# Optimization experiments

Hardware: AMD Instinct MI355X
Metric: run time of the kernel (lower is better)

Reference implementation:

```python
import jax, jax.numpy as jnp
import numpy as np

K = 16  # knn


def conv1x1(x, w, b):
    # x: (B,Cin,k,N), w: (Cout,Cin), b: (Cout,)
    return jnp.einsum('oc,bckn->bokn', w, x) + b[None, :, None, None]


def leaky(x):
    return jnp.where(x >= 0, x, 0.2 * x)


def conv_res(x, sc_w, sc_b, a_w, a_b, b_w, b_b, c_w, c_b):
    sc = conv1x1(x, sc_w, sc_b)
    h = leaky(conv1x1(x, a_w, a_b))
    h = leaky(conv1x1(h, b_w, b_b))
    h = conv1x1(h, c_w, c_b)
    return h + sc


def get_knn_feature(xyz, k):
    # xyz: (B,3,N) -> feature (B,10,k,N)
    x_t = jnp.transpose(xyz, (0, 2, 1))  # (B,N,3)
    xx = jnp.sum(x_t * x_t, axis=-1)  # (B,N)
    inner = jnp.einsum('bnc,bmc->bnm', x_t, x_t)  # (B,N,N)
    d2 = xx[:, :, None] + xx[:, None, :] - 2.0 * inner  # squared dists
    _, idx = jax.lax.top_k(-d2, k)  # (B,N,k) nearest (includes self)
    neighbors = jax.vmap(lambda pts, i: pts[i])(x_t, idx)  # (B,N,k,3)
    center = x_t[:, :, None, :]  # (B,N,1,3)
    rel = neighbors - center
    dist = jnp.sqrt(jnp.sum(rel * rel, axis=-1, keepdims=True) + 1e-12)  # (B,N,k,1)
    feat = jnp.concatenate([jnp.broadcast_to(center, neighbors.shape), neighbors, rel, dist], axis=-1)  # (B,N,k,10)
    return jnp.transpose(feat, (0, 3, 2, 1))  # (B,10,k,N)


def _mk_w(key, o, i):
    s = 1.0 / np.sqrt(i)
    return jax.random.uniform(key, (o, i), jnp.float32, -s, s)


def setup_inputs():
    key = jax.random.key(0)
    ks = jax.random.split(key, 20)
    B, N = 4, 8192
    hide, out = 64, 128
    inp = {'xyz': jax.random.normal(ks[0], (B, 3, N), jnp.float32)}
    # CONV_Res(10, 64, 64)
    inp['p1_sc_w'] = _mk_w(ks[1], hide, 10); inp['p1_sc_b'] = jnp.zeros((hide,), jnp.float32)
    inp['p1_a_w'] = _mk_w(ks[2], hide, 10); inp['p1_a_b'] = jnp.zeros((hide,), jnp.float32)
    inp['p1_b_w'] = _mk_w(ks[3], hide, hide); inp['p1_b_b'] = jnp.zeros((hide,), jnp.float32)
    inp['p1_c_w'] = _mk_w(ks[4], hide, hide); inp['p1_c_b'] = jnp.zeros((hide,), jnp.float32)
    # CONV_Res(128, 64, 128)
    inp['p2_sc_w'] = _mk_w(ks[5], out, 2 * hide); inp['p2_sc_b'] = jnp.zeros((out,), jnp.float32)
    inp['p2_a_w'] = _mk_w(ks[6], hide, 2 * hide); inp['p2_a_b'] = jnp.zeros((hide,), jnp.float32)
    inp['p2_b_w'] = _mk_w(ks[7], out, hide); inp['p2_b_b'] = jnp.zeros((out,), jnp.float32)
    inp['p2_c_w'] = _mk_w(ks[8], out, out); inp['p2_c_b'] = jnp.zeros((out,), jnp.float32)
    return inp


def reference(xyz, p1_sc_w, p1_sc_b, p1_a_w, p1_a_b, p1_b_w, p1_b_b, p1_c_w, p1_c_b,
              p2_sc_w, p2_sc_b, p2_a_w, p2_a_b, p2_b_w, p2_b_b, p2_c_w, p2_c_b):
    x = get_knn_feature(xyz, K)  # (B,10,k,N)
    x = conv_res(x, p1_sc_w, p1_sc_b, p1_a_w, p1_a_b, p1_b_w, p1_b_b, p1_c_w, p1_c_b)  # (B,64,k,N)
    x1 = jnp.max(x, axis=2, keepdims=True)  # (B,64,1,N)
    x1 = jnp.broadcast_to(x1, x.shape)  # repeat over k
    x = jnp.concatenate([x, x1], axis=1)  # (B,128,k,N)
    x = conv_res(x, p2_sc_w, p2_sc_b, p2_a_w, p2_a_b, p2_b_w, p2_b_b, p2_c_w, p2_c_b)  # (B,128,k,N)
    return jnp.max(x, axis=2)  # (B,128,N)
```

## Files before the change

### kernel.cpp

```cpp
#include <hip/hip_runtime.h>
#include <hip/hip_bf16.h>

#define B_ 4
#define N_ 8192
#define KNN 16
#define BN_ (B_*N_)
#define NPOS (BN_*KNN)

typedef __attribute__((ext_vector_type(8))) short bf16x8;
typedef __attribute__((ext_vector_type(4))) float f32x4;

static __device__ __forceinline__ unsigned short f2bf(float f) {
  union { float f; unsigned u; } v; v.f = f;
  unsigned r = v.u + 0x7fff + ((v.u >> 16) & 1);
  return (unsigned short)(r >> 16);
}
static __device__ __forceinline__ float lk(float x) { return x >= 0.f ? x : 0.2f*x; }
static __device__ __forceinline__ unsigned pk2(float a, float b) {
  return (unsigned)f2bf(a) | ((unsigned)f2bf(b) << 16);
}

__global__ void k_prep(const float* __restrict__ xyz, float4* __restrict__ pts4) {
  int i = blockIdx.x * 256 + threadIdx.x;
  if (i >= BN_) return;
  int b = i >> 13, n = i & (N_-1);
  const float* p = xyz + b*3*N_;
  float x = p[n], y = p[N_+n], z = p[2*N_+n];
  float xx = fmaf(z, z, fmaf(y, y, x*x));
  pts4[i] = make_float4(x, y, z, xx);
}

__global__ void k_wcvt(const float* __restrict__ w_sc, const float* __restrict__ w_a,
                       const float* __restrict__ w_b, const float* __restrict__ w_c,
                       const float* __restrict__ p1a, const float* __restrict__ p1sc,
                       const float* __restrict__ p1b, const float* __restrict__ p1c,
                       unsigned short* __restrict__ out) {
  int i = blockIdx.x*256 + threadIdx.x;
  if (i >= 61440) return;
  if (i < 49152) {
    int x = i*2;
    const float* w; int base, K2;
    if (x < 32768)      { w = w_sc; base = 0;     K2 = 256; }
    else if (x < 49152) { w = w_a;  base = 32768; K2 = 256; }
    else if (x < 65536) { w = w_b;  base = 49152; K2 = 128; }
    else                { w = w_c;  base = 65536; K2 = 256; }
    int off = x - base;
    int row = off / K2;
    int colb = (off & (K2-1)) ^ ((row & 7) << 4);
    int k = colb >> 1;
    out[i] = f2bf(w[row*(K2 >> 1) + k]);
  } else {
    int e = i - 49152;
    float val; int byteoff;
    if (e < 2048) {
      int row = e >> 5, k = e & 31;
      val = (k < 10) ? p1a[row*10 + k] : 0.f;
      byteoff = row*64 + ((2*k) ^ ((row & 3) << 4));
    } else if (e < 4096) {
      int le = e - 2048, row = le >> 5, k = le & 31;
      val = (k < 10) ? p1sc[row*10 + k] : 0.f;
      byteoff = 4096 + row*64 + ((2*k) ^ ((row & 3) << 4));
    } else if (e < 8192) {
      int le = e - 4096, row = le >> 6, k = le & 63;
      val = p1b[row*64 + k];
      byteoff = 8192 + row*128 + ((2*k) ^ ((row & 7) << 4));
    } else {
      int le = e - 8192, row = le >> 6, k = le & 63;
      val = p1c[row*64 + k];
      byteoff = 16384 + row*128 + ((2*k) ^ ((row & 7) << 4));
    }
    out[49152 + (byteoff >> 1)] = f2bf(val);
  }
}

static __device__ __forceinline__ unsigned long long bitonic64(
    unsigned long long key, int lane) {
  #pragma unroll
  for (int size = 2; size <= 64; size <<= 1) {
    #pragma unroll
    for (int stride = size >> 1; stride >= 1; stride >>= 1) {
      unsigned long long ok = __shfl_xor((long long)key, stride);
      bool up = ((lane & size) == 0);
      bool keepmin = (((lane & stride) == 0) == up);
      bool oless = ok < key;
      if (oless == keepmin) key = ok;
    }
  }
  return key;
}

template<int U>
static __device__ __forceinline__ void scan_groups(
    const float4* __restrict__ cand, int itbase, int ch,
    float4 me, int lane,
    unsigned long long* __restrict__ bw,
    unsigned long long& topk, float& rhs, int& cnt) {
  float s[U]; int cid[U];
  #pragma unroll
  for (int u = 0; u < U; ++u) {
    int ci = (itbase + u)*64 + lane;
    float4 c = cand[ci];
    float dot = fmaf(me.z, c.z, fmaf(me.y, c.y, me.x*c.x));
    s[u] = fmaf(-2.0f, dot, c.w);
    cid[u] = ch*2048 + ci;
  }
  #pragma unroll
  for (int u = 0; u < U; ++u) {
    unsigned long long m = __ballot(s[u] < rhs);
    if (m) {
      int prefix = __builtin_amdgcn_mbcnt_hi((unsigned)(m >> 32),
                    __builtin_amdgcn_mbcnt_lo((unsigned)m, 0));
      if (s[u] < rhs) {
        float d2 = me.w + s[u];
        bw[cnt + prefix] =
          ((unsigned long long)__float_as_uint(d2) << 32) | (unsigned)cid[u];
      }
      cnt += __popcll(m);
      if (cnt >= 48) {
        int base = 0;
        while (cnt > 0) {
          int c2 = cnt > 48 ? 48 : cnt;
          unsigned long long e = (lane < 16) ? topk
            : ((lane - 16) < c2 ? bw[base + lane - 16] : ~0ull);
          topk = bitonic64(e, lane);
          base += c2; cnt -= c2;
        }
        unsigned long long k15 = __shfl((long long)topk, 15);
        rhs = __uint_as_float((unsigned)(k15 >> 32)) - me.w;
      }
    }
  }
}

__global__ __launch_bounds__(512) void k_knn(const float4* __restrict__ pts4,
                                             int* __restrict__ knn) {
  __shared__ float4 cand[2048];
  __shared__ unsigned long long buf[8][112];
  const int lane = threadIdx.x & 63;
  const int wv   = threadIdx.x >> 6;
  const int q = blockIdx.x * 8 + wv;
  const int b = q >> 13;
  const int n = q & (N_-1);
  const float4* __restrict__ P = pts4 + (b << 13);
  float4 me = P[n];

  unsigned long long topk = ~0ull;
  float rhs = __builtin_inff();
  int cnt = 0;
  unsigned long long* __restrict__ bw = buf[wv];

  for (int ch = 0; ch < 4; ++ch) {
    __syncthreads();
    #pragma unroll
    for (int t = 0; t < 4; ++t)
      cand[t*512 + threadIdx.x] = P[ch*2048 + t*512 + threadIdx.x];
    __syncthreads();

    if (ch == 0) {
      float4 c = cand[lane];
      float dot = fmaf(me.z, c.z, fmaf(me.y, c.y, me.x*c.x));
      float d2 = (me.w + c.w) - 2.0f*dot;
      unsigned long long key =
        ((unsigned long long)__float_as_uint(d2) << 32) | (unsigned)lane;
      topk = bitonic64(key, lane);
      unsigned long long k15 = __shfl((long long)topk, 15);
      rhs = __uint_as_float((unsigned)(k15 >> 32)) - me.w;
      scan_groups<3>(cand, 1, 0, me, lane, bw, topk, rhs, cnt);
      #pragma unroll 1
      for (int it = 4; it < 32; it += 4)
        scan_groups<4>(cand, it, 0, me, lane, bw, topk, rhs, cnt);
    } else {
      #pragma unroll 1
      for (int it = 0; it < 32; it += 4)
        scan_groups<4>(cand, it, ch, me, lane, bw, topk, rhs, cnt);
    }
  }
  {
    int base = 0;
    while (cnt > 0) {
      int c2 = cnt > 48 ? 48 : cnt;
      unsigned long long e = (lane < 16) ? topk
        : ((lane - 16) < c2 ? bw[base + lane - 16] : ~0ull);
      topk = bitonic64(e, lane);
      base += c2; cnt -= c2;
    }
  }
  if (lane < 16) knn[(q << 4) + lane] = (int)(unsigned)(topk & 0xffffffffu);
}

__global__ __launch_bounds__(512, 2) void k_p12(
    const float4* __restrict__ pts4, const int* __restrict__ knn,
    const unsigned short* __restrict__ wbf,
    const float* __restrict__ a_b1, const float* __restrict__ b_b1,
    const float* __restrict__ c_b1, const float* __restrict__ sc_b1,
    const float* __restrict__ sc_b2, const float* __restrict__ a_b2,
    const float* __restrict__ b_b2, const float* __restrict__ c_b2,
    float* __restrict__ out) {
  __shared__ __align__(16) unsigned short Ws1[12288];
  __shared__ __align__(16) unsigned short Ws2[49152];
  __shared__ __align__(16) unsigned short Hr[8][2304];
  const int tid = threadIdx.x;
  const int lane = tid & 63, wv = tid >> 6;
  const int colr = lane & 15, kq = lane >> 4;

  #pragma unroll
  for (int j = 0; j < 3; ++j)
    ((uint4*)Ws1)[j*512 + tid] = ((const uint4*)(wbf + 49152))[j*512 + tid];
  #pragma unroll
  for (int it = 0; it < 12; ++it)
    ((uint4*)Ws2)[it*512 + tid] = ((const uint4*)wbf)[it*512 + tid];

  const char* WS = (const char*)Ws1;
  const char* WSC = (const char*)Ws2;
  const char* WA  = (const char*)(Ws2 + 16384);
  const char* WB  = (const char*)(Ws2 + 24576);
  const char* WC  = (const char*)(Ws2 + 32768);
  char* H = (char*)Hr[wv];
  float (*outT)[16] = (float(*)[16])(&Hr[0][0]);

#define WF(base, row, K2, ksbyte) \
  (*(const bf16x8*)((base) + (row)*(K2) + ((((ksbyte) + kq*16)) ^ (((row)&7)<<4))))

  __syncthreads();

  for (int t = 0; t < 8; ++t) {
    const int bn0 = blockIdx.x*128 + t*16;

    unsigned short fb0[10], fb1[10];
    #pragma unroll
    for (int ct = 0; ct < 2; ++ct) {
      int bn = bn0 + wv*2 + ct;
      int b = bn >> 13;
      float4 cp = pts4[bn];
      int nid = knn[bn*16 + colr];
      float4 np = pts4[(b << 13) + nid];
      float rx = np.x - cp.x, ry = np.y - cp.y, rz = np.z - cp.z;
      float dist = sqrtf(fmaf(rz, rz, fmaf(ry, ry, rx*rx)) + 1e-12f);
      unsigned short* fb = ct ? fb1 : fb0;
      fb[0]=f2bf(cp.x); fb[1]=f2bf(cp.y); fb[2]=f2bf(cp.z);
      fb[3]=f2bf(np.x); fb[4]=f2bf(np.y); fb[5]=f2bf(np.z);
      fb[6]=f2bf(rx);   fb[7]=f2bf(ry);   fb[8]=f2bf(rz);   fb[9]=f2bf(dist);
    }
    bf16x8 bfr[2];
    #pragma unroll
    for (int ct = 0; ct < 2; ++ct) {
      const unsigned short* fb = ct ? fb1 : fb0;
      #pragma unroll
      for (int j = 0; j < 8; ++j) {
        unsigned short v1 = (j < 2) ? fb[8+j] : (unsigned short)0;
        unsigned short e = (kq == 0) ? fb[j] : ((kq == 1) ? v1 : (unsigned short)0);
        bfr[ct][j] = (short)e;
      }
    }

    f32x4 acc1[4][2];
    #pragma unroll
    for (int mt = 0; mt < 4; ++mt) {
      int r0 = mt*16 + kq*4;
      #pragma unroll
      for (int r = 0; r < 4; ++r) {
        float bia = c_b1[r0+r] + sc_b1[r0+r];
        acc1[mt][0][r] = bia; acc1[mt][1][r] = bia;
      }
    }
    #pragma unroll
    for (int mt = 0; mt < 4; ++mt) {
      int row = mt*16 + colr;
      bf16x8 w = *(const bf16x8*)(WS + 4096 + row*64 + ((kq*16) ^ ((row&3)<<4)));
      acc1[mt][0] = __builtin_amdgcn_mfma_f32_16x16x32_bf16(w, bfr[0], acc1[mt][0], 0, 0, 0);
      acc1[mt][1] = __builtin_amdgcn_mfma_f32_16x16x32_bf16(w, bfr[1], acc1[mt][1], 0, 0, 0);
    }

    f32x4 ha[4][2];
    #pragma unroll
    for (int mt = 0; mt < 4; ++mt) {
      int r0 = mt*16 + kq*4;
      #pragma unroll
      for (int r = 0; r < 4; ++r) { ha[mt][0][r] = a_b1[r0+r]; ha[mt][1][r] = a_b1[r0+r]; }
    }
    #pragma unroll
    for (int mt = 0; mt < 4; ++mt) {
      int row = mt*16 + colr;
      bf16x8 w = *(const bf16x8*)(WS + row*64 + ((kq*16) ^ ((row&3)<<4)));
      ha[mt][0] = __builtin_amdgcn_mfma_f32_16x16x32_bf16(w, bfr[0], ha[mt][0], 0, 0, 0);
      ha[mt][1] = __builtin_amdgcn_mfma_f32_16x16x32_bf16(w, bfr[1], ha[mt][1], 0, 0, 0);
    }

    #pragma unroll
    for (int mt = 0; mt < 4; ++mt) {
      int ch2 = (mt*16 + kq*4) * 2;
      #pragma unroll
      for (int ct = 0; ct < 2; ++ct) {
        int posl = ct*16 + colr;
        uint2 u;
        u.x = pk2(lk(ha[mt][ct][0]), lk(ha[mt][ct][1]));
        u.y = pk2(lk(ha[mt][ct][2]), lk(ha[mt][ct][3]));
        *(uint2*)(H + posl*128 + (ch2 ^ ((posl&7)<<4))) = u;
      }
    }
    bf16x8 bh1[2][2];
    #pragma unroll
    for (int ct = 0; ct < 2; ++ct) {
      int posl = ct*16 + colr;
      #pragma unroll
      for (int k2 = 0; k2 < 2; ++k2)
        bh1[ct][k2] = *(const bf16x8*)(H + posl*128 + ((k2*64 + kq*16) ^ ((posl&7)<<4)));
    }

    #pragma unroll
    for (int jj = 0; jj < 2; ++jj) {
      f32x4 h2[2][2];
      #pragma unroll
      for (int mtp = 0; mtp < 2; ++mtp) {
        int r0 = (jj*2 + mtp)*16 + kq*4;
        #pragma unroll
        for (int r = 0; r < 4; ++r) { h2[mtp][0][r] = b_b1[r0+r]; h2[mtp][1][r] = b_b1[r0+r]; }
      }
      #pragma unroll
      for (int mtp = 0; mtp < 2; ++mtp) {
        int row = (jj*2 + mtp)*16 + colr;
        #pragma unroll
        for (int k2 = 0; k2 < 2; ++k2) {
          bf16x8 w = *(const bf16x8*)(WS + 8192 + row*128 + ((k2*64 + kq*16) ^ ((row&7)<<4)));
          h2[mtp][0] = __builtin_amdgcn_mfma_f32_16x16x32_bf16(w, bh1[0][k2], h2[mtp][0], 0, 0, 0);
          h2[mtp][1] = __builtin_amdgcn_mfma_f32_16x16x32_bf16(w, bh1[1][k2], h2[mtp][1], 0, 0, 0);
        }
      }
      #pragma unroll
      for (int mtp = 0; mtp < 2; ++mtp) {
        int ch2 = ((jj*2 + mtp)*16 + kq*4) * 2;
        #pragma unroll
        for (int ct = 0; ct < 2; ++ct) {
          int posl = ct*16 + colr;
          uint2 u;
          u.x = pk2(lk(h2[mtp][ct][0]), lk(h2[mtp][ct][1]));
          u.y = pk2(lk(h2[mtp][ct][2]), lk(h2[mtp][ct][3]));
          *(uint2*)(H + posl*128 + (ch2 ^ ((posl&7)<<4))) = u;
        }
      }
      bf16x8 b2[2];
      #pragma unroll
      for (int ct = 0; ct < 2; ++ct) {
        int posl = ct*16 + colr;
        b2[ct] = *(const bf16x8*)(H + posl*128 + ((jj*64 + kq*16) ^ ((posl&7)<<4)));
      }
      #pragma unroll
      for (int mt = 0; mt < 4; ++mt) {
        int row = mt*16 + colr;
        bf16x8 w = *(const bf16x8*)(WS + 16384 + row*128 + ((jj*64 + kq*16) ^ ((row&7)<<4)));
        acc1[mt][0] = __builtin_amdgcn_mfma_f32_16x16x32_bf16(w, b2[0], acc1[mt][0], 0, 0, 0);
        acc1[mt][1] = __builtin_amdgcn_mfma_f32_16x16x32_bf16(w, b2[1], acc1[mt][1], 0, 0, 0);
      }
    }

    #pragma unroll
    for (int ct = 0; ct < 2; ++ct) {
      int posl = ct*16 + colr;
      #pragma unroll
      for (int mt = 0; mt < 4; ++mt) {
        int ch0 = mt*16 + kq*4;
        uint2 u;
        u.x = pk2(acc1[mt][ct][0], acc1[mt][ct][1]);
        u.y = pk2(acc1[mt][ct][2], acc1[mt][ct][3]);
        *(uint2*)(H + ((posl*128 + ch0*2) ^ ((posl&7)<<4))) = u;
        float m[4];
        #pragma unroll
        for (int r = 0; r < 4; ++r) {
          float v = acc1[mt][ct][r];
          v = fmaxf(v, __shfl_xor(v, 1));
          v = fmaxf(v, __shfl_xor(v, 2));
          v = fmaxf(v, __shfl_xor(v, 4));
          v = fmaxf(v, __shfl_xor(v, 8));
          m[r] = v;
        }
        if (colr == 0) {
          uint2 um; um.x = pk2(m[0], m[1]); um.y = pk2(m[2], m[3]);
          *(uint2*)(H + 4096 + ct*128 + ch0*2) = um;
        }
      }
    }

    bf16x8 bx[2][4];
    #pragma unroll
    for (int ct = 0; ct < 2; ++ct) {
      int posl = ct*16 + colr;
      bx[ct][0] = *(const bf16x8*)(H + ((posl*128 + kq*16) ^ ((posl&7)<<4)));
      bx[ct][1] = *(const bf16x8*)(H + ((posl*128 + 64 + kq*16) ^ ((posl&7)<<4)));
      bx[ct][2] = *(const bf16x8*)(H + 4096 + ct*128 + kq*16);
      bx[ct][3] = *(const bf16x8*)(H + 4096 + ct*128 + 64 + kq*16);
    }

    f32x4 acc[8][2];
    #pragma unroll
    for (int mt = 0; mt < 8; ++mt) {
      int r0 = mt*16 + kq*4;
      #pragma unroll
      for (int r = 0; r < 4; ++r) {
        float bia = c_b2[r0+r] + sc_b2[r0+r];
        acc[mt][0][r] = bia; acc[mt][1][r] = bia;
      }
    }
    #pragma unroll
    for (int mt = 0; mt < 8; ++mt) {
      int row = mt*16 + colr;
      #pragma unroll
      for (int ks = 0; ks < 4; ++ks) {
        bf16x8 w = WF(WSC, row, 256, ks*64);
        acc[mt][0] = __builtin_amdgcn_mfma_f32_16x16x32_bf16(w, bx[0][ks], acc[mt][0], 0, 0, 0);
        acc[mt][1] = __builtin_amdgcn_mfma_f32_16x16x32_bf16(w, bx[1][ks], acc[mt][1], 0, 0, 0);
      }
    }

    f32x4 ha2[4][2];
    #pragma unroll
    for (int mt = 0; mt < 4; ++mt) {
      int r0 = mt*16 + kq*4;
      #pragma unroll
      for (int r = 0; r < 4; ++r) { ha2[mt][0][r] = a_b2[r0+r]; ha2[mt][1][r] = a_b2[r0+r]; }
    }
    #pragma unroll
    for (int mt = 0; mt < 4; ++mt) {
      int row = mt*16 + colr;
      #pragma unroll
      for (int ks = 0; ks < 4; ++ks) {
        bf16x8 w = WF(WA, row, 256, ks*64);
        ha2[mt][0] = __builtin_amdgcn_mfma_f32_16x16x32_bf16(w, bx[0][ks], ha2[mt][0], 0, 0, 0);
        ha2[mt][1] = __builtin_amdgcn_mfma_f32_16x16x32_bf16(w, bx[1][ks], ha2[mt][1], 0, 0, 0);
      }
    }

    #pragma unroll
    for (int mt = 0; mt < 4; ++mt) {
      int ch2 = (mt*16 + kq*4) * 2;
      #pragma unroll
      for (int ct = 0; ct < 2; ++ct) {
        int posl = ct*16 + colr;
        uint2 u;
        u.x = pk2(lk(ha2[mt][ct][0]), lk(ha2[mt][ct][1]));
        u.y = pk2(lk(ha2[mt][ct][2]), lk(ha2[mt][ct][3]));
        *(uint2*)(H + posl*128 + (ch2 ^ ((posl&7)<<4))) = u;
      }
    }
    bf16x8 bh[2][2];
    #pragma unroll
    for (int ct = 0; ct < 2; ++ct) {
      int posl = ct*16 + colr;
      #pragma unroll
      for (int k2 = 0; k2 < 2; ++k2)
        bh[ct][k2] = *(const bf16x8*)(H + posl*128 + ((k2*64 + kq*16) ^ ((posl&7)<<4)));
    }

    #pragma unroll
    for (int j = 0; j < 4; ++j) {
      f32x4 h2[2][2];
      #pragma unroll
      for (int mtp = 0; mtp < 2; ++mtp) {
        int r0 = (2*j + mtp)*16 + kq*4;
        #pragma unroll
        for (int r = 0; r < 4; ++r) { h2[mtp][0][r] = b_b2[r0+r]; h2[mtp][1][r] = b_b2[r0+r]; }
      }
      #pragma unroll
      for (int mtp = 0; mtp < 2; ++mtp) {
        int row = (2*j + mtp)*16 + colr;
        #pragma unroll
        for (int k2 = 0; k2 < 2; ++k2) {
          bf16x8 w = WF(WB, row, 128, k2*64);
          h2[mtp][0] = __builtin_amdgcn_mfma_f32_16x16x32_bf16(w, bh[0][k2], h2[mtp][0], 0, 0, 0);
          h2[mtp][1] = __builtin_amdgcn_mfma_f32_16x16x32_bf16(w, bh[1][k2], h2[mtp][1], 0, 0, 0);
        }
      }
      char* PB = H + (j & 1)*2048;
      #pragma unroll
      for (int mtp = 0; mtp < 2; ++mtp) {
        int chp2 = (mtp*16 + kq*4) * 2;
        #pragma unroll
        for (int ct = 0; ct < 2; ++ct) {
          int posl = ct*16 + colr;
          uint2 u;
          u.x = pk2(lk(h2[mtp][ct][0]), lk(h2[mtp][ct][1]));
          u.y = pk2(lk(h2[mtp][ct][2]), lk(h2[mtp][ct][3]));
          *(uint2*)(PB + posl*64 + (chp2 ^ ((posl&3)<<4))) = u;
        }
      }
      bf16x8 b2[2];
      #pragma unroll
      for (int ct = 0; ct < 2; ++ct) {
        int posl = ct*16 + colr;
        b2[ct] = *(const bf16x8*)(PB + posl*64 + ((kq*16) ^ ((posl&3)<<4)));
      }
      #pragma unroll
      for (int mt = 0; mt < 8; ++mt) {
        int row = mt*16 + colr;
        bf16x8 w = WF(WC, row, 256, j*64);
        acc[mt][0] = __builtin_amdgcn_mfma_f32_16x16x32_bf16(w, b2[0], acc[mt][0], 0, 0, 0);
        acc[mt][1] = __builtin_amdgcn_mfma_f32_16x16x32_bf16(w, b2[1], acc[mt][1], 0, 0, 0);
      }
    }

    __syncthreads();
    #pragma unroll
    for (int mt = 0; mt < 8; ++mt) {
      #pragma unroll
      for (int ct = 0; ct < 2; ++ct) {
        #pragma unroll
        for (int r = 0; r < 4; ++r) {
          float v = acc[mt][ct][r];
          v = fmaxf(v, __shfl_xor(v, 1));
          v = fmaxf(v, __shfl_xor(v, 2));
          v = fmaxf(v, __shfl_xor(v, 4));
          v = fmaxf(v, __shfl_xor(v, 8));
          if (colr == 0) outT[mt*16 + kq*4 + r][wv*2 + ct] = v;
        }
      }
    }
    __syncthreads();
    {
      int ch = tid >> 2, p = tid & 3;
      int b = bn0 >> 13, n0 = bn0 & (N_-1);
      float4 v4 = *(const float4*)&outT[ch][p*4];
      *(float4*)(out + ((size_t)b*128 + ch)*N_ + n0 + p*4) = v4;
    }
    __syncthreads();
  }
#undef WF
}

extern "C" void kernel_launch(void* const* d_in, const int* in_sizes, int n_in,
                              void* d_out, int out_size, void* d_ws, size_t ws_size,
                              hipStream_t stream) {
  const float* xyz     = (const float*)d_in[0];
  const float* p1_sc_w = (const float*)d_in[1];
  const float* p1_sc_b = (const float*)d_in[2];
  const float* p1_a_w  = (const float*)d_in[3];
  const float* p1_a_b  = (const float*)d_in[4];
  const float* p1_b_w  = (const float*)d_in[5];
  const float* p1_b_b  = (const float*)d_in[6];
  const float* p1_c_w  = (const float*)d_in[7];
  const float* p1_c_b  = (const float*)d_in[8];
  const float* p2_sc_w = (const float*)d_in[9];
  const float* p2_sc_b = (const float*)d_in[10];
  const float* p2_a_w  = (const float*)d_in[11];
  const float* p2_a_b  = (const float*)d_in[12];
  const float* p2_b_w  = (const float*)d_in[13];
  const float* p2_b_b  = (const float*)d_in[14];
  const float* p2_c_w  = (const float*)d_in[15];
  const float* p2_c_b  = (const float*)d_in[16];

  if (ws_size < 75497472u) return;
  char* ws = (char*)d_ws;
  float4* pts4        = (float4*)(ws);
  unsigned short* wbf = (unsigned short*)(ws + 524288);
  int* knn            = (int*)(ws + 655360);
  float* out = (float*)d_out;

  k_prep<<<dim3(BN_/256), dim3(256), 0, stream>>>(xyz, pts4);
  k_wcvt<<<dim3(240), dim3(256), 0, stream>>>(p2_sc_w, p2_a_w, p2_b_w, p2_c_w,
      p1_a_w, p1_sc_w, p1_b_w, p1_c_w, wbf);
  k_knn<<<dim3(BN_/8), dim3(512), 0, stream>>>(pts4, knn);
  k_p12<<<dim3(256), dim3(512), 0, stream>>>(pts4, knn, wbf,
      p1_a_b, p1_b_b, p1_c_b, p1_sc_b,
      p2_sc_b, p2_a_b, p2_b_b, p2_c_b, out);
}
```

Baseline: 379.5 us.

## Process one point per wave in k_p12 with 1024-thread blocks

Doubles the block size of the fused MLP kernel to 16 waves, so each wave handles a single point's 16 neighbours instead of two. Per-wave accumulators and staging buffers are halved, which cuts register pressure and is meant to raise occupancy and hide latency. In exchange each weight fragment read from LDS feeds only one MFMA instead of two, so LDS weight traffic per FLOP doubles. The __launch_bounds__(1024,4) hint may also be unreachable given the LDS footprint.

```diff
diff --git a/kernel.cpp b/kernel.cpp
--- a/kernel.cpp
+++ b/kernel.cpp
@@ -188,7 +188,7 @@
   if (lane < 16) knn[(q << 4) + lane] = (int)(unsigned)(topk & 0xffffffffu);
 }
 
-__global__ __launch_bounds__(512, 2) void k_p12(
+__global__ __launch_bounds__(1024, 4) void k_p12(
     const float4* __restrict__ pts4, const int* __restrict__ knn,
     const unsigned short* __restrict__ wbf,
     const float* __restrict__ a_b1, const float* __restrict__ b_b1,
@@ -198,17 +198,19 @@
     float* __restrict__ out) {
   __shared__ __align__(16) unsigned short Ws1[12288];
   __shared__ __align__(16) unsigned short Ws2[49152];
-  __shared__ __align__(16) unsigned short Hr[8][2304];
+  __shared__ __align__(16) unsigned short Hr[16][1152];
   const int tid = threadIdx.x;
   const int lane = tid & 63, wv = tid >> 6;
   const int colr = lane & 15, kq = lane >> 4;
 
   #pragma unroll
-  for (int j = 0; j < 3; ++j)
-    ((uint4*)Ws1)[j*512 + tid] = ((const uint4*)(wbf + 49152))[j*512 + tid];
+  for (int j = 0; j < 2; ++j) {
+    int c = j*1024 + tid;
+    if (c < 1536) ((uint4*)Ws1)[c] = ((const uint4*)(wbf + 49152))[c];
+  }
   #pragma unroll
-  for (int it = 0; it < 12; ++it)
-    ((uint4*)Ws2)[it*512 + tid] = ((const uint4*)wbf)[it*512 + tid];
+  for (int it = 0; it < 6; ++it)
+    ((uint4*)Ws2)[it*1024 + tid] = ((const uint4*)wbf)[it*1024 + tid];
 
   const char* WS = (const char*)Ws1;
   const char* WSC = (const char*)Ws2;
@@ -225,96 +227,77 @@
 
   for (int t = 0; t < 8; ++t) {
     const int bn0 = blockIdx.x*128 + t*16;
-
-    unsigned short fb0[10], fb1[10];
-    #pragma unroll
-    for (int ct = 0; ct < 2; ++ct) {
-      int bn = bn0 + wv*2 + ct;
+    const int bn = bn0 + wv;
+
+    unsigned short fb[10];
+    {
       int b = bn >> 13;
       float4 cp = pts4[bn];
       int nid = knn[bn*16 + colr];
       float4 np = pts4[(b << 13) + nid];
       float rx = np.x - cp.x, ry = np.y - cp.y, rz = np.z - cp.z;
       float dist = sqrtf(fmaf(rz, rz, fmaf(ry, ry, rx*rx)) + 1e-12f);
-      unsigned short* fb = ct ? fb1 : fb0;
       fb[0]=f2bf(cp.x); fb[1]=f2bf(cp.y); fb[2]=f2bf(cp.z);
       fb[3]=f2bf(np.x); fb[4]=f2bf(np.y); fb[5]=f2bf(np.z);
       fb[6]=f2bf(rx);   fb[7]=f2bf(ry);   fb[8]=f2bf(rz);   fb[9]=f2bf(dist);
     }
-    bf16x8 bfr[2];
-    #pragma unroll
-    for (int ct = 0; ct < 2; ++ct) {
-      const unsigned short* fb = ct ? fb1 : fb0;
-      #pragma unroll
-      for (int j = 0; j < 8; ++j) {
-        unsigned short v1 = (j < 2) ? fb[8+j] : (unsigned short)0;
-        unsigned short e = (kq == 0) ? fb[j] : ((kq == 1) ? v1 : (unsigned short)0);
-        bfr[ct][j] = (short)e;
-      }
-    }
-
-    f32x4 acc1[4][2];
+    bf16x8 bfr;
+    #pragma unroll
+    for (int j = 0; j < 8; ++j) {
+      unsigned short v1 = (j < 2) ? fb[8+j] : (unsigned short)0;
+      unsigned short e = (kq == 0) ? fb[j] : ((kq == 1) ? v1 : (unsigned short)0);
+      bfr[j] = (short)e;
+    }
+
+    f32x4 acc1[4];
     #pragma unroll
     for (int mt = 0; mt < 4; ++mt) {
       int r0 = mt*16 + kq*4;
       #pragma unroll
-      for (int r = 0; r < 4; ++r) {
-        float bia = c_b1[r0+r] + sc_b1[r0+r];
-        acc1[mt][0][r] = bia; acc1[mt][1][r] = bia;
-      }
+      for (int r = 0; r < 4; ++r) acc1[mt][r] = c_b1[r0+r] + sc_b1[r0+r];
     }
     #pragma unroll
     for (int mt = 0; mt < 4; ++mt) {
       int row = mt*16 + colr;
       bf16x8 w = *(const bf16x8*)(WS + 4096 + row*64 + ((kq*16) ^ ((row&3)<<4)));
-      acc1[mt][0] = __builtin_amdgcn_mfma_f32_16x16x32_bf16(w, bfr[0], acc1[mt][0], 0, 0, 0);
-      acc1[mt][1] = __builtin_amdgcn_mfma_f32_16x16x32_bf16(w, bfr[1], acc1[mt][1], 0, 0, 0);
-    }
-
-    f32x4 ha[4][2];
+      acc1[mt] = __builtin_amdgcn_mfma_f32_16x16x32_bf16(w, bfr, acc1[mt], 0, 0, 0);
+    }
+
+    f32x4 ha[4];
     #pragma unroll
     for (int mt = 0; mt < 4; ++mt) {
       int r0 = mt*16 + kq*4;
       #pragma unroll
-      for (int r = 0; r < 4; ++r) { ha[mt][0][r] = a_b1[r0+r]; ha[mt][1][r] = a_b1[r0+r]; }
+      for (int r = 0; r < 4; ++r) ha[mt][r] = a_b1[r0+r];
     }
     #pragma unroll
     for (int mt = 0; mt < 4; ++mt) {
       int row = mt*16 + colr;
       bf16x8 w = *(const bf16x8*)(WS + row*64 + ((kq*16) ^ ((row&3)<<4)));
-      ha[mt][0] = __builtin_amdgcn_mfma_f32_16x16x32_bf16(w, bfr[0], ha[mt][0], 0, 0, 0);
-      ha[mt][1] = __builtin_amdgcn_mfma_f32_16x16x32_bf16(w, bfr[1], ha[mt][1], 0, 0, 0);
+      ha[mt] = __builtin_amdgcn_mfma_f32_16x16x32_bf16(w, bfr, ha[mt], 0, 0, 0);
     }
 
     #pragma unroll
     for (int mt = 0; mt < 4; ++mt) {
       int ch2 = (mt*16 + kq*4) * 2;
-      #pragma unroll
-      for (int ct = 0; ct < 2; ++ct) {
-        int posl = ct*16 + colr;
-        uint2 u;
-        u.x = pk2(lk(ha[mt][ct][0]), lk(ha[mt][ct][1]));
-        u.y = pk2(lk(ha[mt][ct][2]), lk(ha[mt][ct][3]));
-        *(uint2*)(H + posl*128 + (ch2 ^ ((posl&7)<<4))) = u;
-      }
-    }
-    bf16x8 bh1[2][2];
-    #pragma unroll
-    for (int ct = 0; ct < 2; ++ct) {
-      int posl = ct*16 + colr;
-      #pragma unroll
-      for (int k2 = 0; k2 < 2; ++k2)
-        bh1[ct][k2] = *(const bf16x8*)(H + posl*128 + ((k2*64 + kq*16) ^ ((posl&7)<<4)));
-    }
+      uint2 u;
+      u.x = pk2(lk(ha[mt][0]), lk(ha[mt][1]));
+      u.y = pk2(lk(ha[mt][2]), lk(ha[mt][3]));
+      *(uint2*)(H + colr*128 + (ch2 ^ ((colr&7)<<4))) = u;
+    }
+    bf16x8 bh1[2];
+    #pragma unroll
+    for (int k2 = 0; k2 < 2; ++k2)
+      bh1[k2] = *(const bf16x8*)(H + colr*128 + ((k2*64 + kq*16) ^ ((colr&7)<<4)));
 
     #pragma unroll
     for (int jj = 0; jj < 2; ++jj) {
-      f32x4 h2[2][2];
+      f32x4 h2[2];
       #pragma unroll
       for (int mtp = 0; mtp < 2; ++mtp) {
         int r0 = (jj*2 + mtp)*16 + kq*4;
         #pragma unroll
-        for (int r = 0; r < 4; ++r) { h2[mtp][0][r] = b_b1[r0+r]; h2[mtp][1][r] = b_b1[r0+r]; }
+        for (int r = 0; r < 4; ++r) h2[mtp][r] = b_b1[r0+r];
       }
       #pragma unroll
       for (int mtp = 0; mtp < 2; ++mtp) {
@@ -322,83 +305,61 @@
         #pragma unroll
         for (int k2 = 0; k2 < 2; ++k2) {
           bf16x8 w = *(const bf16x8*)(WS + 8192 + row*128 + ((k2*64 + kq*16) ^ ((row&7)<<4)));
-          h2[mtp][0] = __builtin_amdgcn_mfma_f32_16x16x32_bf16(w, bh1[0][k2], h2[mtp][0], 0, 0, 0);
-          h2[mtp][1] = __builtin_amdgcn_mfma_f32_16x16x32_bf16(w, bh1[1][k2], h2[mtp][1], 0, 0, 0);
+          h2[mtp] = __builtin_amdgcn_mfma_f32_16x16x32_bf16(w, bh1[k2], h2[mtp], 0, 0, 0);
         }
       }
       #pragma unroll
       for (int mtp = 0; mtp < 2; ++mtp) {
         int ch2 = ((jj*2 + mtp)*16 + kq*4) * 2;
-        #pragma unroll
-        for (int ct = 0; ct < 2; ++ct) {
-          int posl = ct*16 + colr;
-          uint2 u;
-          u.x = pk2(lk(h2[mtp][ct][0]), lk(h2[mtp][ct][1]));
-          u.y = pk2(lk(h2[mtp][ct][2]), lk(h2[mtp][ct][3]));
-          *(uint2*)(H + posl*128 + (ch2 ^ ((posl&7)<<4))) = u;
-        }
-      }
-      bf16x8 b2[2];
-      #pragma unroll
-      for (int ct = 0; ct < 2; ++ct) {
-        int posl = ct*16 + colr;
-        b2[ct] = *(const bf16x8*)(H + posl*128 + ((jj*64 + kq*16) ^ ((posl&7)<<4)));
-      }
+        uint2 u;
+        u.x = pk2(lk(h2[mtp][0]), lk(h2[mtp][1]));
+        u.y = pk2(lk(h2[mtp][2]), lk(h2[mtp][3]));
+        *(uint2*)(H + colr*128 + (ch2 ^ ((colr&7)<<4))) = u;
+      }
+      bf16x8 b2 = *(const bf16x8*)(H + colr*128 + ((jj*64 + kq*16) ^ ((colr&7)<<4)));
       #pragma unroll
       for (int mt = 0; mt < 4; ++mt) {
         int row = mt*16 + colr;
         bf16x8 w = *(const bf16x8*)(WS + 16384 + row*128 + ((jj*64 + kq*16) ^ ((row&7)<<4)));
-        acc1[mt][0] = __builtin_amdgcn_mfma_f32_16x16x32_bf16(w, b2[0], acc1[mt][0], 0, 0, 0);
-        acc1[mt][1] = __builtin_amdgcn_mfma_f32_16x16x32_bf16(w, b2[1], acc1[mt][1], 0, 0, 0);
-      }
-    }
-
-    #pragma unroll
-    for (int ct = 0; ct < 2; ++ct) {
-      int posl = ct*16 + colr;
-      #pragma unroll
-      for (int mt = 0; mt < 4; ++mt) {
-        int ch0 = mt*16 + kq*4;
-        uint2 u;
-        u.x = pk2(acc1[mt][ct][0], acc1[mt][ct][1]);
-        u.y = pk2(acc1[mt][ct][2], acc1[mt][ct][3]);
-        *(uint2*)(H + ((posl*128 + ch0*2) ^ ((posl&7)<<4))) = u;
-        float m[4];
-        #pragma unroll
-        for (int r = 0; r < 4; ++r) {
-          float v = acc1[mt][ct][r];
-          v = fmaxf(v, __shfl_xor(v, 1));
-          v = fmaxf(v, __shfl_xor(v, 2));
-          v = fmaxf(v, __shfl_xor(v, 4));
-          v = fmaxf(v, __shfl_xor(v, 8));
-          m[r] = v;
-        }
-        if (colr == 0) {
-          uint2 um; um.x = pk2(m[0], m[1]); um.y = pk2(m[2], m[3]);
-          *(uint2*)(H + 4096 + ct*128 + ch0*2) = um;
-        }
-      }
-    }
-
-    bf16x8 bx[2][4];
-    #pragma unroll
-    for (int ct = 0; ct < 2; ++ct) {
-      int posl = ct*16 + colr;
-      bx[ct][0] = *(const bf16x8*)(H + ((posl*128 + kq*16) ^ ((posl&7)<<4)));
-      bx[ct][1] = *(const bf16x8*)(H + ((posl*128 + 64 + kq*16) ^ ((posl&7)<<4)));
-      bx[ct][2] = *(const bf16x8*)(H + 4096 + ct*128 + kq*16);
-      bx[ct][3] = *(const bf16x8*)(H + 4096 + ct*128 + 64 + kq*16);
-    }
-
-    f32x4 acc[8][2];
+        acc1[mt] = __builtin_amdgcn_mfma_f32_16x16x32_bf16(w, b2, acc1[mt], 0, 0, 0);
+      }
+    }
+
+    #pragma unroll
+    for (int mt = 0; mt < 4; ++mt) {
+      int ch0 = mt*16 + kq*4;
+      uint2 u;
+      u.x = pk2(acc1[mt][0], acc1[mt][1]);
+      u.y = pk2(acc1[mt][2], acc1[mt][3]);
+      *(uint2*)(H + colr*128 + ((ch0*2) ^ ((colr&7)<<4))) = u;
+      float m[4];
+      #pragma unroll
+      for (int r = 0; r < 4; ++r) {
+        float v = acc1[mt][r];
+        v = fmaxf(v, __shfl_xor(v, 1));
+        v = fmaxf(v, __shfl_xor(v, 2));
+        v = fmaxf(v, __shfl_xor(v, 4));
+        v = fmaxf(v, __shfl_xor(v, 8));
+        m[r] = v;
+      }
+      if (colr == 0) {
+        uint2 um; um.x = pk2(m[0], m[1]); um.y = pk2(m[2], m[3]);
+        *(uint2*)(H + 2048 + ch0*2) = um;
+      }
+    }
+
+    bf16x8 bx[4];
+    bx[0] = *(const bf16x8*)(H + colr*128 + ((kq*16) ^ ((colr&7)<<4)));
+    bx[1] = *(const bf16x8*)(H + colr*128 + ((64 + kq*16) ^ ((colr&7)<<4)));
+    bx[2] = *(const bf16x8*)(H + 2048 + kq*16);
+    bx[3] = *(const bf16x8*)(H + 2048 + 64 + kq*16);
+
+    f32x4 acc[8];
     #pragma unroll
     for (int mt = 0; mt < 8; ++mt) {
       int r0 = mt*16 + kq*4;
       #pragma unroll
-      for (int r = 0; r < 4; ++r) {
-        float bia = c_b2[r0+r] + sc_b2[r0+r];
-        acc[mt][0][r] = bia; acc[mt][1][r] = bia;
-      }
+      for (int r = 0; r < 4; ++r) acc[mt][r] = c_b2[r0+r] + sc_b2[r0+r];
     }
     #pragma unroll
     for (int mt = 0; mt < 8; ++mt) {
@@ -406,17 +367,16 @@
       #pragma unroll
       for (int ks = 0; ks < 4; ++ks) {
         bf16x8 w = WF(WSC, row, 256, ks*64);
-        acc[mt][0] = __builtin_amdgcn_mfma_f32_16x16x32_bf16(w, bx[0][ks], acc[mt][0], 0, 0, 0);
-        acc[mt][1] = __builtin_amdgcn_mfma_f32_16x16x32_bf16(w, bx[1][ks], acc[mt][1], 0, 0, 0);
-      }
-    }
-
-    f32x4 ha2[4][2];
+        acc[mt] = __builtin_amdgcn_mfma_f32_16x16x32_bf16(w, bx[ks], acc[mt], 0, 0, 0);
+      }
+    }
+
+    f32x4 ha2[4];
     #pragma unroll
     for (int mt = 0; mt < 4; ++mt) {
       int r0 = mt*16 + kq*4;
       #pragma unroll
-      for (int r = 0; r < 4; ++r) { ha2[mt][0][r] = a_b2[r0+r]; ha2[mt][1][r] = a_b2[r0+r]; }
+      for (int r = 0; r < 4; ++r) ha2[mt][r] = a_b2[r0+r];
     }
     #pragma unroll
     for (int mt = 0; mt < 4; ++mt) {
@@ -424,40 +384,31 @@
       #pragma unroll
       for (int ks = 0; ks < 4; ++ks) {
         bf16x8 w = WF(WA, row, 256, ks*64);
-        ha2[mt][0] = __builtin_amdgcn_mfma_f32_16x16x32_bf16(w, bx[0][ks], ha2[mt][0], 0, 0, 0);
-        ha2[mt][1] = __builtin_amdgcn_mfma_f32_16x16x32_bf16(w, bx[1][ks], ha2[mt][1], 0, 0, 0);
+        ha2[mt] = __builtin_amdgcn_mfma_f32_16x16x32_bf16(w, bx[ks], ha2[mt], 0, 0, 0);
       }
     }
 
     #pragma unroll
     for (int mt = 0; mt < 4; ++mt) {
       int ch2 = (mt*16 + kq*4) * 2;
-      #pragma unroll
-      for (int ct = 0; ct < 2; ++ct) {
-        int posl = ct*16 + colr;
-        uint2 u;
-        u.x = pk2(lk(ha2[mt][ct][0]), lk(ha2[mt][ct][1]));
-        u.y = pk2(lk(ha2[mt][ct][2]), lk(ha2[mt][ct][3]));
-        *(uint2*)(H + posl*128 + (ch2 ^ ((posl&7)<<4))) = u;
-      }
-    }
-    bf16x8 bh[2][2];
-    #pragma unroll
-    for (int ct = 0; ct < 2; ++ct) {
-      int posl = ct*16 + colr;
-      #pragma unroll
-      for (int k2 = 0; k2 < 2; ++k2)
-        bh[ct][k2] = *(const bf16x8*)(H + posl*128 + ((k2*64 + kq*16) ^ ((posl&7)<<4)));
-    }
+      uint2 u;
+      u.x = pk2(lk(ha2[mt][0]), lk(ha2[mt][1]));
+      u.y = pk2(lk(ha2[mt][2]), lk(ha2[mt][3]));
+      *(uint2*)(H + colr*128 + (ch2 ^ ((colr&7)<<4))) = u;
+    }
+    bf16x8 bh[2];
+    #pragma unroll
+    for (int k2 = 0; k2 < 2; ++k2)
+      bh[k2] = *(const bf16x8*)(H + colr*128 + ((k2*64 + kq*16) ^ ((colr&7)<<4)));
 
     #pragma unroll
     for (int j = 0; j < 4; ++j) {
-      f32x4 h2[2][2];
+      f32x4 h2[2];
       #pragma unroll
       for (int mtp = 0; mtp < 2; ++mtp) {
         int r0 = (2*j + mtp)*16 + kq*4;
         #pragma unroll
-        for (int r = 0; r < 4; ++r) { h2[mtp][0][r] = b_b2[r0+r]; h2[mtp][1][r] = b_b2[r0+r]; }
+        for (int r = 0; r < 4; ++r) h2[mtp][r] = b_b2[r0+r];
       }
       #pragma unroll
       for (int mtp = 0; mtp < 2; ++mtp) {
@@ -465,35 +416,24 @@
         #pragma unroll
         for (int k2 = 0; k2 < 2; ++k2) {
           bf16x8 w = WF(WB, row, 128, k2*64);
-          h2[mtp][0] = __builtin_amdgcn_mfma_f32_16x16x32_bf16(w, bh[0][k2], h2[mtp][0], 0, 0, 0);
-          h2[mtp][1] = __builtin_amdgcn_mfma_f32_16x16x32_bf16(w, bh[1][k2], h2[mtp][1], 0, 0, 0);
+          h2[mtp] = __builtin_amdgcn_mfma_f32_16x16x32_bf16(w, bh[k2], h2[mtp], 0, 0, 0);
         }
       }
-      char* PB = H + (j & 1)*2048;
+      char* PB = H + (j & 1)*1024;
       #pragma unroll
       for (int mtp = 0; mtp < 2; ++mtp) {
         int chp2 = (mtp*16 + kq*4) * 2;
-        #pragma unroll
-        for (int ct = 0; ct < 2; ++ct) {
-          int posl = ct*16 + colr;
-          uint2 u;
-          u.x = pk2(lk(h2[mtp][ct][0]), lk(h2[mtp][ct][1]));
-          u.y = pk2(lk(h2[mtp][ct][2]), lk(h2[mtp][ct][3]));
-          *(uint2*)(PB + posl*64 + (chp2 ^ ((posl&3)<<4))) = u;
-        }
-      }
-      bf16x8 b2[2];
-      #pragma unroll
-      for (int ct = 0; ct < 2; ++ct) {
-        int posl = ct*16 + colr;
-        b2[ct] = *(const bf16x8*)(PB + posl*64 + ((kq*16) ^ ((posl&3)<<4)));
-      }
+        uint2 u;
+        u.x = pk2(lk(h2[mtp][0]), lk(h2[mtp][1]));
+        u.y = pk2(lk(h2[mtp][2]), lk(h2[mtp][3]));
+        *(uint2*)(PB + colr*64 + (chp2 ^ ((colr&3)<<4))) = u;
+      }
+      bf16x8 b2 = *(const bf16x8*)(PB + colr*64 + ((kq*16) ^ ((colr&3)<<4)));
       #pragma unroll
       for (int mt = 0; mt < 8; ++mt) {
         int row = mt*16 + colr;
         bf16x8 w = WF(WC, row, 256, j*64);
-        acc[mt][0] = __builtin_amdgcn_mfma_f32_16x16x32_bf16(w, b2[0], acc[mt][0], 0, 0, 0);
-        acc[mt][1] = __builtin_amdgcn_mfma_f32_16x16x32_bf16(w, b2[1], acc[mt][1], 0, 0, 0);
+        acc[mt] = __builtin_amdgcn_mfma_f32_16x16x32_bf16(w, b2, acc[mt], 0, 0, 0);
       }
     }
 
@@ -501,20 +441,17 @@
     #pragma unroll
     for (int mt = 0; mt < 8; ++mt) {
       #pragma unroll
-      for (int ct = 0; ct < 2; ++ct) {
-        #pragma unroll
-        for (int r = 0; r < 4; ++r) {
-          float v = acc[mt][ct][r];
-          v = fmaxf(v, __shfl_xor(v, 1));
-          v = fmaxf(v, __shfl_xor(v, 2));
-          v = fmaxf(v, __shfl_xor(v, 4));
-          v = fmaxf(v, __shfl_xor(v, 8));
-          if (colr == 0) outT[mt*16 + kq*4 + r][wv*2 + ct] = v;
-        }
+      for (int r = 0; r < 4; ++r) {
+        float v = acc[mt][r];
+        v = fmaxf(v, __shfl_xor(v, 1));
+        v = fmaxf(v, __shfl_xor(v, 2));
+        v = fmaxf(v, __shfl_xor(v, 4));
+        v = fmaxf(v, __shfl_xor(v, 8));
+        if (colr == 0) outT[mt*16 + kq*4 + r][wv] = v;
       }
     }
     __syncthreads();
-    {
+    if (tid < 512) {
       int ch = tid >> 2, p = tid & 3;
       int b = bn0 >> 13, n0 = bn0 & (N_-1);
       float4 v4 = *(const float4*)&outT[ch][p*4];
@@ -557,7 +494,7 @@
   k_wcvt<<<dim3(240), dim3(256), 0, stream>>>(p2_sc_w, p2_a_w, p2_b_w, p2_c_w,
       p1_a_w, p1_sc_w, p1_b_w, p1_c_w, wbf);
   k_knn<<<dim3(BN_/8), dim3(512), 0, stream>>>(pts4, knn);
-  k_p12<<<dim3(256), dim3(512), 0, stream>>>(pts4, knn, wbf,
+  k_p12<<<dim3(256), dim3(1024), 0, stream>>>(pts4, knn, wbf,
       p1_a_b, p1_b_b, p1_c_b, p1_sc_b,
       p2_sc_b, p2_a_b, p2_b_b, p2_c_b, out);
 }
```

Result: slower. 409.4 us (+7.9%).
